# Performance work log

Hardware: AMD Instinct MI355X
Metric: run time of the kernel (lower is better)

## Reference

```python
import jax, jax.numpy as jnp
import numpy as np

B, S, D, H = 2, 2048, 1024, 16
HD = D // H
MASK_VALUE = -1000000.0


def setup_inputs() -> dict:
    key = jax.random.key(0)
    ks = jax.random.split(key, 8)
    scale = 1.0 / np.sqrt(D)
    return {
        "Q": jax.random.normal(ks[0], (B, S, D), jnp.float32),
        "K": jax.random.normal(ks[1], (B, S, D), jnp.float32),
        "V": jax.random.normal(ks[2], (B, S, D), jnp.float32),
        "valid_lens": jax.random.randint(ks[3], (B,), 0, S).astype(jnp.int32),
        "Wq": jax.random.normal(ks[4], (D, D), jnp.float32) * scale,
        "Wk": jax.random.normal(ks[5], (D, D), jnp.float32) * scale,
        "Wv": jax.random.normal(ks[6], (D, D), jnp.float32) * scale,
        "Wo": jax.random.normal(ks[7], (D, D), jnp.float32) * scale,
    }


def _split_heads(x):
    # [B,S,D] -> [B,H,S,HD]
    return x.reshape(B, S, H, HD).transpose(0, 2, 1, 3)


def reference(Q, K, V, valid_lens, Wq, Wk, Wv, Wo):
    q = _split_heads(Q @ Wq)
    k = _split_heads(K @ Wk)
    v = _split_heads(V @ Wv)
    # scores: [B,H,Sq,Sk]
    scores = jnp.einsum("bhqd,bhkd->bhqk", q, k) / jnp.sqrt(jnp.float32(HD))
    # mask key positions >= valid_len (per batch, broadcast over heads/queries)
    key_pos = jnp.arange(S)  # [Sk]
    mask = key_pos[None, None, None, :] < valid_lens[:, None, None, None]
    scores = jnp.where(mask, scores, MASK_VALUE)
    attn = jax.nn.softmax(scores, axis=-1)
    out = jnp.einsum("bhqk,bhkd->bhqd", attn, v)  # [B,H,S,HD]
    out = out.transpose(0, 2, 1, 3).reshape(B, S, D)
    return out @ Wo
```

## Files before the change

kernel.cpp:

```cpp
#include <hip/hip_runtime.h>
#include <stdint.h>

#define B_ 2
#define S_ 2048
#define D_ 1024
#define H_ 16
#define HD_ 64
#define MG_ (B_*S_)
#define MASKV -1000000.0f
#define LP_ 72
#define LO_ 68
#define M2_ 17.3f

typedef __bf16 bf16;
typedef bf16 bf16x8 __attribute__((ext_vector_type(8)));
typedef bf16 bf16x4 __attribute__((ext_vector_type(4)));
typedef float f32x4 __attribute__((ext_vector_type(4)));

#define MFMA(a, b, c) __builtin_amdgcn_mfma_f32_16x16x32_bf16(a, b, c, 0, 0, 0)

__device__ __forceinline__ void gl_lds16(const bf16* g, bf16* l) {
  __builtin_amdgcn_global_load_lds((const __attribute__((address_space(1))) void*)g,
                                   (__attribute__((address_space(3))) void*)l, 16, 0, 0);
}

__global__ __launch_bounds__(256) void wcast_kernel(const float* __restrict__ W0, const float* __restrict__ W1,
                                                    const float* __restrict__ W2, const float* __restrict__ W3,
                                                    bf16* __restrict__ T) {
  const float* W = blockIdx.z == 0 ? W0 : blockIdx.z == 1 ? W1 : blockIdx.z == 2 ? W2 : W3;
  bf16* Tz = T + (size_t)blockIdx.z * D_ * D_;
  __shared__ float tile[32][33];
  int tx = threadIdx.x & 31, ty = threadIdx.x >> 5;
  int bn = blockIdx.x * 32, bk = blockIdx.y * 32;
#pragma unroll
  for (int i = 0; i < 32; i += 8)
    tile[ty + i][tx] = W[(size_t)(bk + ty + i) * D_ + bn + tx];
  __syncthreads();
#pragma unroll
  for (int i = 0; i < 32; i += 8)
    Tz[(size_t)(bn + ty + i) * D_ + bk + tx] = (bf16)tile[tx][ty + i];
}

__global__ __launch_bounds__(256) void proj_gemm(const float* __restrict__ Qin, const float* __restrict__ Kin,
                                                 const float* __restrict__ Vin, const bf16* __restrict__ WT,
                                                 bf16* __restrict__ qh, bf16* __restrict__ kh,
                                                 bf16* __restrict__ vT) {
  __shared__ alignas(16) bf16 Asf[128 * 32];
  __shared__ alignas(16) bf16 Ash[128 * 32];
  int mode = blockIdx.y;
  int bx = blockIdx.x;
  int i1 = (bx & 7) + ((bx >> 6) << 3);
  int i2 = (bx >> 3) & 7;
  int tid = threadIdx.x, lane = tid & 63, w = tid >> 6;
  int wm = w >> 1, wn = w & 1, ml = lane & 15, quad = lane >> 4;
  int rr = tid >> 3, c4 = (tid & 7) * 4;
  int l4 = lane >> 2, k8 = (lane & 3) * 8;
  f32x4 acc[4][4] = {};

  const float* Fp = mode == 0 ? Qin : mode == 1 ? Kin : Vin;
  const bf16* Hp = WT + (size_t)mode * D_ * D_;
  int frow0 = i1 * 128, hrow0 = i2 * 128;
  bf16* Xs = (mode < 2) ? Asf : Ash;
  bf16* Ys = (mode < 2) ? Ash : Asf;

  for (int kk = 0; kk < D_; kk += 32) {
    __syncthreads();
#pragma unroll
    for (int j = 0; j < 2; ++j) {
      int chunk = w * 2 + j;
      gl_lds16(&Hp[(size_t)(hrow0 + chunk * 16 + l4) * D_ + kk + k8], &Ash[chunk * 16 * 32]);
    }
#pragma unroll
    for (int p = 0; p < 4; ++p) {
      float4 v = *(const float4*)&Fp[(size_t)(frow0 + rr + p * 32) * D_ + kk + c4];
      bf16x4 bv; bv[0] = (bf16)v.x; bv[1] = (bf16)v.y; bv[2] = (bf16)v.z; bv[3] = (bf16)v.w;
      *(bf16x4*)&Asf[(rr + p * 32) * 32 + c4] = bv;
    }
    __syncthreads();
    bf16x8 af[4], bfr[4];
#pragma unroll
    for (int mt = 0; mt < 4; ++mt) af[mt] = *(bf16x8*)&Xs[(wm * 64 + mt * 16 + ml) * 32 + quad * 8];
#pragma unroll
    for (int nt = 0; nt < 4; ++nt) bfr[nt] = *(bf16x8*)&Ys[(wn * 64 + nt * 16 + ml) * 32 + quad * 8];
#pragma unroll
    for (int mt = 0; mt < 4; ++mt)
#pragma unroll
      for (int nt = 0; nt < 4; ++nt)
        acc[mt][nt] = MFMA(af[mt], bfr[nt], acc[mt][nt]);
  }

  if (mode < 2) {
    bf16* dst = mode ? kh : qh;
    float oscale = mode ? 1.0f : 0.125f * 1.44269504088896f;
    int m0 = i1 * 128, n0 = i2 * 128;
#pragma unroll
    for (int mt = 0; mt < 4; ++mt)
#pragma unroll
      for (int nt = 0; nt < 4; ++nt)
#pragma unroll
        for (int r = 0; r < 4; ++r) {
          int m = m0 + wm * 64 + mt * 16 + quad * 4 + r;
          int n = n0 + wn * 64 + nt * 16 + ml;
          int b = m >> 11, s = m & (S_ - 1), h = n >> 6, hd = n & 63;
          dst[(((size_t)(b * H_ + h)) * S_ + s) * HD_ + hd] = (bf16)(acc[mt][nt][r] * oscale);
        }
  } else {
    int m0 = i2 * 128, n0 = i1 * 128;
#pragma unroll
    for (int mt = 0; mt < 4; ++mt)
#pragma unroll
      for (int nt = 0; nt < 4; ++nt)
#pragma unroll
        for (int r = 0; r < 4; ++r) {
          int dcol = m0 + wm * 64 + mt * 16 + quad * 4 + r;
          int n = n0 + wn * 64 + nt * 16 + ml;
          int b = n >> 11, s = n & (S_ - 1), h = dcol >> 6, hd = dcol & 63;
          vT[(((size_t)(b * H_ + h)) * HD_ + hd) * S_ + s] = (bf16)acc[mt][nt][r];
        }
  }
}

__global__ __launch_bounds__(256) void attn_kernel(const bf16* __restrict__ qh, const bf16* __restrict__ kh,
                                                   const bf16* __restrict__ vT, const int* __restrict__ vlen,
                                                   bf16* __restrict__ ctx) {
  __shared__ alignas(16) char ldsraw[35328];
  bf16* Ps = (bf16*)ldsraw;
  float* Om = (float*)ldsraw;
  float* Lv = (float*)(ldsraw + 34816);

  int tid = threadIdx.x, lane = tid & 63, w = tid >> 6;
  int ml = lane & 15, quad = lane >> 4;
  int wq = w >> 1, wk = w & 1;
  int bx = blockIdx.x;
  int bh = (bx & 7) + ((bx >> 8) << 3);
  int qt = (bx >> 3) & 31;
  int b = bh >> 4, h = bh & 15;
  const bf16* qbase = qh + ((size_t)bh * S_ + qt * 64 + wq * 32) * HD_;
  const bf16* kbase = kh + (size_t)bh * S_ * HD_;
  const bf16* vbase = vT + (size_t)bh * HD_ * S_;
  int valid = vlen[b];
  int nkt = (valid == 0) ? (S_ / 64) : ((valid + 63) >> 6);

  bf16x8 aq[2][2];
#pragma unroll
  for (int mt = 0; mt < 2; ++mt)
#pragma unroll
    for (int half = 0; half < 2; ++half)
      aq[mt][half] = *(const bf16x8*)&qbase[(mt * 16 + ml) * HD_ + half * 32 + quad * 8];

  bf16 onev = (bf16)1.0f;
  bf16x8 ones = {onev, onev, onev, onev, onev, onev, onev, onev};

  f32x4 o[2][4] = {};
  f32x4 lacc[2] = {};

  bf16* Pw = Ps + (size_t)w * 32 * LP_;

  for (int kt = wk; kt < nkt; kt += 2) {
    const bf16* kp = kbase + (size_t)kt * 64 * HD_;
    bool tail = (kt * 64 + 64 > valid);
    bf16x8 bk[4][2];
#pragma unroll
    for (int nt = 0; nt < 4; ++nt)
#pragma unroll
      for (int half = 0; half < 2; ++half)
        bk[nt][half] = *(const bf16x8*)&kp[(nt * 16 + ml) * HD_ + half * 32 + quad * 8];

#pragma unroll
    for (int mt = 0; mt < 2; ++mt) {
      f32x4 sc[4];
#pragma unroll
      for (int nt = 0; nt < 4; ++nt) {
        f32x4 c = {};
        c = MFMA(aq[mt][0], bk[nt][0], c);
        c = MFMA(aq[mt][1], bk[nt][1], c);
        sc[nt] = c;
      }
#pragma unroll
      for (int r = 0; r < 4; ++r) {
#pragma unroll
        for (int nt = 0; nt < 4; ++nt) {
          float s = sc[nt][r];
          if (tail) {
            int col = kt * 64 + nt * 16 + ml;
            if (col >= valid) s = MASKV;
          }
          if (valid == 0) s = 0.f;
          float p = exp2f(s - M2_);
          Pw[(mt * 16 + quad * 4 + r) * LP_ + nt * 16 + ml] = (bf16)p;
        }
      }
    }
#pragma unroll
    for (int ks = 0; ks < 2; ++ks) {
      bf16x8 bv[4];
#pragma unroll
      for (int ht = 0; ht < 4; ++ht)
        bv[ht] = *(const bf16x8*)&vbase[(size_t)(ht * 16 + ml) * S_ + kt * 64 + ks * 32 + quad * 8];
#pragma unroll
      for (int mt = 0; mt < 2; ++mt) {
        bf16x8 ap = *(bf16x8*)&Pw[(mt * 16 + ml) * LP_ + ks * 32 + quad * 8];
        lacc[mt] = MFMA(ap, ones, lacc[mt]);
#pragma unroll
        for (int ht = 0; ht < 4; ++ht) o[mt][ht] = MFMA(ap, bv[ht], o[mt][ht]);
      }
    }
  }

  __syncthreads();
#pragma unroll
  for (int mt = 0; mt < 2; ++mt) {
#pragma unroll
    for (int r = 0; r < 4; ++r) {
      int rl = mt * 16 + quad * 4 + r;
#pragma unroll
      for (int ht = 0; ht < 4; ++ht)
        Om[(w * 32 + rl) * LO_ + ht * 16 + ml] = o[mt][ht][r];
      if (ml == 0) Lv[w * 32 + rl] = lacc[mt][r];
    }
  }
  __syncthreads();
#pragma unroll 4
  for (int rr = 0; rr < 16; ++rr) {
    int rg = w * 16 + rr;
    int wqs = rg >> 5, rl = rg & 31;
    int s0 = (wqs * 2) * 32 + rl, s1 = (wqs * 2 + 1) * 32 + rl;
    float ls = Lv[s0] + Lv[s1];
    float ov = Om[s0 * LO_ + lane] + Om[s1 * LO_ + lane];
    ctx[((size_t)b * S_ + qt * 64 + rg) * D_ + h * 64 + lane] = (bf16)(ov / ls);
  }
}

__global__ __launch_bounds__(256) void out_gemm(const bf16* __restrict__ ctx, const bf16* __restrict__ WoT,
                                                float* __restrict__ out) {
  __shared__ alignas(16) bf16 As[128 * 32];
  __shared__ alignas(16) bf16 Bs[64 * 32];
  int bx = blockIdx.x;
  int mt8 = (bx & 7) + ((bx >> 7) << 3);
  int ntile = (bx >> 3) & 15;
  int tid = threadIdx.x, lane = tid & 63, w = tid >> 6;
  int wm = w >> 1, wn = w & 1, ml = lane & 15, quad = lane >> 4;
  int l4 = lane >> 2, k8 = (lane & 3) * 8;
  int m0 = mt8 * 128, n0 = ntile * 64;
  f32x4 acc[4][2] = {};
  for (int kk = 0; kk < D_; kk += 32) {
    __syncthreads();
#pragma unroll
    for (int j = 0; j < 2; ++j) {
      int chunk = w * 2 + j;
      gl_lds16(&ctx[(size_t)(m0 + chunk * 16 + l4) * D_ + kk + k8], &As[chunk * 16 * 32]);
    }
    gl_lds16(&WoT[(size_t)(n0 + w * 16 + l4) * D_ + kk + k8], &Bs[w * 16 * 32]);
    __syncthreads();
    bf16x8 af[4], bfr[2];
#pragma unroll
    for (int mt = 0; mt < 4; ++mt) af[mt] = *(bf16x8*)&As[(wm * 64 + mt * 16 + ml) * 32 + quad * 8];
#pragma unroll
    for (int nt = 0; nt < 2; ++nt) bfr[nt] = *(bf16x8*)&Bs[(wn * 32 + nt * 16 + ml) * 32 + quad * 8];
#pragma unroll
    for (int mt = 0; mt < 4; ++mt)
#pragma unroll
      for (int nt = 0; nt < 2; ++nt)
        acc[mt][nt] = MFMA(af[mt], bfr[nt], acc[mt][nt]);
  }
#pragma unroll
  for (int mt = 0; mt < 4; ++mt)
#pragma unroll
    for (int nt = 0; nt < 2; ++nt)
#pragma unroll
      for (int r = 0; r < 4; ++r) {
        int m = m0 + wm * 64 + mt * 16 + quad * 4 + r;
        int n = n0 + wn * 32 + nt * 16 + ml;
        out[(size_t)m * D_ + n] = acc[mt][nt][r];
      }
}

extern "C" void kernel_launch(void* const* d_in, const int* in_sizes, int n_in,
                              void* d_out, int out_size, void* d_ws, size_t ws_size,
                              hipStream_t stream) {
  const float* Q = (const float*)d_in[0];
  const float* K = (const float*)d_in[1];
  const float* V = (const float*)d_in[2];
  const int* vl = (const int*)d_in[3];
  const float* Wq = (const float*)d_in[4];
  const float* Wk = (const float*)d_in[5];
  const float* Wv = (const float*)d_in[6];
  const float* Wo = (const float*)d_in[7];
  char* ws = (char*)d_ws;
  bf16* WT  = (bf16*)ws;
  bf16* qh  = (bf16*)(ws + 8ull * 1024 * 1024);
  bf16* kh  = (bf16*)(ws + 16ull * 1024 * 1024);
  bf16* vT  = (bf16*)(ws + 24ull * 1024 * 1024);
  bf16* ctx = (bf16*)(ws + 32ull * 1024 * 1024);
  float* out = (float*)d_out;

  wcast_kernel<<<dim3(32, 32, 4), 256, 0, stream>>>(Wq, Wk, Wv, Wo, WT);
  proj_gemm<<<dim3(256, 3), 256, 0, stream>>>(Q, K, V, WT, qh, kh, vT);
  attn_kernel<<<dim3(1024), 256, 0, stream>>>(qh, kh, vT, vl, ctx);
  out_gemm<<<dim3(512), 256, 0, stream>>>(ctx, WT + 3ull * D_ * D_, out);
}
```

Before: 233.2 us.

## Load-balance attention across batches with persistent blocks and 4-way key split

Blocks are split between the two batches in proportion to their valid key-tile counts, and each block loops persistently over (head, 32-row query tile) work units. All four waves now share the same query rows and split the key tiles four ways, with a 4-way LDS reduction at the end of each unit. The intent is to stop blocks for the short-valid batch idling while blocks for the long-valid batch are still running. In exchange the kernel adds extra barriers per work unit and a larger reduction, and it relies on gridDim being chosen by the launcher, which is not shown here.

```diff
diff --git a/kernel.cpp b/kernel.cpp
--- a/kernel.cpp
+++ b/kernel.cpp
@@ -130,104 +130,115 @@
 
   int tid = threadIdx.x, lane = tid & 63, w = tid >> 6;
   int ml = lane & 15, quad = lane >> 4;
-  int wq = w >> 1, wk = w & 1;
+  int wk = w;
+
+  int v0 = vlen[0], v1 = vlen[1];
+  int n0 = (v0 == 0) ? (S_ / 64) : ((v0 + 63) >> 6);
+  int n1 = (v1 == 0) ? (S_ / 64) : ((v1 + 63) >> 6);
+  int G = gridDim.x;
+  int G0 = (int)(((long)G * n0 + ((n0 + n1) >> 1)) / (n0 + n1));
+  G0 = G0 < 1 ? 1 : (G0 > G - 1 ? G - 1 : G0);
   int bx = blockIdx.x;
-  int bh = (bx & 7) + ((bx >> 8) << 3);
-  int qt = (bx >> 3) & 31;
-  int b = bh >> 4, h = bh & 15;
-  const bf16* qbase = qh + ((size_t)bh * S_ + qt * 64 + wq * 32) * HD_;
-  const bf16* kbase = kh + (size_t)bh * S_ * HD_;
-  const bf16* vbase = vT + (size_t)bh * HD_ * S_;
-  int valid = vlen[b];
-  int nkt = (valid == 0) ? (S_ / 64) : ((valid + 63) >> 6);
-
-  bf16x8 aq[2][2];
-#pragma unroll
-  for (int mt = 0; mt < 2; ++mt)
-#pragma unroll
-    for (int half = 0; half < 2; ++half)
-      aq[mt][half] = *(const bf16x8*)&qbase[(mt * 16 + ml) * HD_ + half * 32 + quad * 8];
+  int b, ustart, ustep;
+  if (bx < G0) { b = 0; ustart = bx; ustep = G0; }
+  else         { b = 1; ustart = bx - G0; ustep = G - G0; }
+  int valid = b ? v1 : v0;
+  int nkt = b ? n1 : n0;
 
   bf16 onev = (bf16)1.0f;
   bf16x8 ones = {onev, onev, onev, onev, onev, onev, onev, onev};
-
-  f32x4 o[2][4] = {};
-  f32x4 lacc[2] = {};
-
   bf16* Pw = Ps + (size_t)w * 32 * LP_;
 
-  for (int kt = wk; kt < nkt; kt += 2) {
-    const bf16* kp = kbase + (size_t)kt * 64 * HD_;
-    bool tail = (kt * 64 + 64 > valid);
-    bf16x8 bk[4][2];
-#pragma unroll
-    for (int nt = 0; nt < 4; ++nt)
+  for (int u = ustart; u < 1024; u += ustep) {
+    int h = u & 15, qt = u >> 4;
+    int bh = (b << 4) | h;
+    const bf16* qbase = qh + ((size_t)bh * S_ + qt * 32) * HD_;
+    const bf16* kbase = kh + (size_t)bh * S_ * HD_;
+    const bf16* vbase = vT + (size_t)bh * HD_ * S_;
+
+    bf16x8 aq[2][2];
+#pragma unroll
+    for (int mt = 0; mt < 2; ++mt)
 #pragma unroll
       for (int half = 0; half < 2; ++half)
-        bk[nt][half] = *(const bf16x8*)&kp[(nt * 16 + ml) * HD_ + half * 32 + quad * 8];
-
+        aq[mt][half] = *(const bf16x8*)&qbase[(mt * 16 + ml) * HD_ + half * 32 + quad * 8];
+
+    f32x4 o[2][4] = {};
+    f32x4 lacc[2] = {};
+
+    for (int kt = wk; kt < nkt; kt += 4) {
+      const bf16* kp = kbase + (size_t)kt * 64 * HD_;
+      bool tail = (kt * 64 + 64 > valid);
+      bf16x8 bk[4][2];
+#pragma unroll
+      for (int nt = 0; nt < 4; ++nt)
+#pragma unroll
+        for (int half = 0; half < 2; ++half)
+          bk[nt][half] = *(const bf16x8*)&kp[(nt * 16 + ml) * HD_ + half * 32 + quad * 8];
+
+#pragma unroll
+      for (int mt = 0; mt < 2; ++mt) {
+        f32x4 sc[4];
+#pragma unroll
+        for (int nt = 0; nt < 4; ++nt) {
+          f32x4 c = {};
+          c = MFMA(aq[mt][0], bk[nt][0], c);
+          c = MFMA(aq[mt][1], bk[nt][1], c);
+          sc[nt] = c;
+        }
+#pragma unroll
+        for (int r = 0; r < 4; ++r) {
+#pragma unroll
+          for (int nt = 0; nt < 4; ++nt) {
+            float s = sc[nt][r];
+            if (tail) {
+              int col = kt * 64 + nt * 16 + ml;
+              if (col >= valid) s = MASKV;
+            }
+            if (valid == 0) s = 0.f;
+            float p = exp2f(s - M2_);
+            Pw[(mt * 16 + quad * 4 + r) * LP_ + nt * 16 + ml] = (bf16)p;
+          }
+        }
+      }
+#pragma unroll
+      for (int ks = 0; ks < 2; ++ks) {
+        bf16x8 bv[4];
+#pragma unroll
+        for (int ht = 0; ht < 4; ++ht)
+          bv[ht] = *(const bf16x8*)&vbase[(size_t)(ht * 16 + ml) * S_ + kt * 64 + ks * 32 + quad * 8];
+#pragma unroll
+        for (int mt = 0; mt < 2; ++mt) {
+          bf16x8 ap = *(bf16x8*)&Pw[(mt * 16 + ml) * LP_ + ks * 32 + quad * 8];
+          lacc[mt] = MFMA(ap, ones, lacc[mt]);
+#pragma unroll
+          for (int ht = 0; ht < 4; ++ht) o[mt][ht] = MFMA(ap, bv[ht], o[mt][ht]);
+        }
+      }
+    }
+
+    __syncthreads();
 #pragma unroll
     for (int mt = 0; mt < 2; ++mt) {
-      f32x4 sc[4];
-#pragma unroll
-      for (int nt = 0; nt < 4; ++nt) {
-        f32x4 c = {};
-        c = MFMA(aq[mt][0], bk[nt][0], c);
-        c = MFMA(aq[mt][1], bk[nt][1], c);
-        sc[nt] = c;
+#pragma unroll
+      for (int r = 0; r < 4; ++r) {
+        int rl = mt * 16 + quad * 4 + r;
+#pragma unroll
+        for (int ht = 0; ht < 4; ++ht)
+          Om[(w * 32 + rl) * LO_ + ht * 16 + ml] = o[mt][ht][r];
+        if (ml == 0) Lv[w * 32 + rl] = lacc[mt][r];
       }
-#pragma unroll
-      for (int r = 0; r < 4; ++r) {
-#pragma unroll
-        for (int nt = 0; nt < 4; ++nt) {
-          float s = sc[nt][r];
-          if (tail) {
-            int col = kt * 64 + nt * 16 + ml;
-            if (col >= valid) s = MASKV;
-          }
-          if (valid == 0) s = 0.f;
-          float p = exp2f(s - M2_);
-          Pw[(mt * 16 + quad * 4 + r) * LP_ + nt * 16 + ml] = (bf16)p;
-        }
-      }
-    }
-#pragma unroll
-    for (int ks = 0; ks < 2; ++ks) {
-      bf16x8 bv[4];
-#pragma unroll
-      for (int ht = 0; ht < 4; ++ht)
-        bv[ht] = *(const bf16x8*)&vbase[(size_t)(ht * 16 + ml) * S_ + kt * 64 + ks * 32 + quad * 8];
-#pragma unroll
-      for (int mt = 0; mt < 2; ++mt) {
-        bf16x8 ap = *(bf16x8*)&Pw[(mt * 16 + ml) * LP_ + ks * 32 + quad * 8];
-        lacc[mt] = MFMA(ap, ones, lacc[mt]);
-#pragma unroll
-        for (int ht = 0; ht < 4; ++ht) o[mt][ht] = MFMA(ap, bv[ht], o[mt][ht]);
-      }
-    }
-  }
-
-  __syncthreads();
-#pragma unroll
-  for (int mt = 0; mt < 2; ++mt) {
-#pragma unroll
-    for (int r = 0; r < 4; ++r) {
-      int rl = mt * 16 + quad * 4 + r;
-#pragma unroll
-      for (int ht = 0; ht < 4; ++ht)
-        Om[(w * 32 + rl) * LO_ + ht * 16 + ml] = o[mt][ht][r];
-      if (ml == 0) Lv[w * 32 + rl] = lacc[mt][r];
-    }
-  }
-  __syncthreads();
-#pragma unroll 4
-  for (int rr = 0; rr < 16; ++rr) {
-    int rg = w * 16 + rr;
-    int wqs = rg >> 5, rl = rg & 31;
-    int s0 = (wqs * 2) * 32 + rl, s1 = (wqs * 2 + 1) * 32 + rl;
-    float ls = Lv[s0] + Lv[s1];
-    float ov = Om[s0 * LO_ + lane] + Om[s1 * LO_ + lane];
-    ctx[((size_t)b * S_ + qt * 64 + rg) * D_ + h * 64 + lane] = (bf16)(ov / ls);
+    }
+    __syncthreads();
+#pragma unroll
+    for (int rr = 0; rr < 8; ++rr) {
+      int rl = w * 8 + rr;
+      float ls = Lv[rl] + Lv[32 + rl] + Lv[64 + rl] + Lv[96 + rl];
+      float ov = Om[rl * LO_ + lane] + Om[(32 + rl) * LO_ + lane] +
+                 Om[(64 + rl) * LO_ + lane] + Om[(96 + rl) * LO_ + lane];
+      ctx[((size_t)b * S_ + qt * 32 + rl) * D_ + h * 64 + lane] = (bf16)(ov / ls);
+    }
+    __syncthreads();
   }
 }
 
```

New measurement: 283.7 us. +21.6%, slower.

## Skip K/V projection tiles beyond valid length and async-load fp32 tokens

Applied to the files above, without the earlier changes.

The K and V projection GEMM blocks now return early when their token rows lie past the rounded-up valid length, since attention never reads those keys or values. The fp32 token tiles are loaded straight into LDS with global_load_lds and converted to bf16 when the MFMA fragments are read, replacing the register load, convert and LDS store path. The valid==0 case now zeroes Q fragments instead of doing a per-element branch in the softmax loop. This cuts projection work in proportion to the padding and shortens the load path, at the cost of twice the LDS for the fp32 tile and extra conversion work during fragment reads.

```diff
diff --git a/kernel.cpp b/kernel.cpp
--- a/kernel.cpp
+++ b/kernel.cpp
@@ -11,6 +11,7 @@
 #define LP_ 72
 #define LO_ 68
 #define M2_ 17.3f
+#define QSCALE_ (0.125f * 1.44269504088896f)
 
 typedef __bf16 bf16;
 typedef bf16 bf16x8 __attribute__((ext_vector_type(8)));
@@ -19,9 +20,22 @@
 
 #define MFMA(a, b, c) __builtin_amdgcn_mfma_f32_16x16x32_bf16(a, b, c, 0, 0, 0)
 
-__device__ __forceinline__ void gl_lds16(const bf16* g, bf16* l) {
+__device__ __forceinline__ void gl_lds16(const void* g, void* l) {
   __builtin_amdgcn_global_load_lds((const __attribute__((address_space(1))) void*)g,
                                    (__attribute__((address_space(3))) void*)l, 16, 0, 0);
+}
+
+__device__ __forceinline__ bf16x8 ldcvt8(const float* p) {
+  float4 a = *(const float4*)p;
+  float4 b = *(const float4*)(p + 4);
+  bf16x8 r;
+  r[0] = (bf16)a.x; r[1] = (bf16)a.y; r[2] = (bf16)a.z; r[3] = (bf16)a.w;
+  r[4] = (bf16)b.x; r[5] = (bf16)b.y; r[6] = (bf16)b.z; r[7] = (bf16)b.w;
+  return r;
+}
+
+__device__ __forceinline__ int kneed_of(int valid) {
+  return (valid == 0) ? S_ : ((valid + 63) & ~63);
 }
 
 __global__ __launch_bounds__(256) void wcast_kernel(const float* __restrict__ W0, const float* __restrict__ W1,
@@ -44,44 +58,53 @@
 __global__ __launch_bounds__(256) void proj_gemm(const float* __restrict__ Qin, const float* __restrict__ Kin,
                                                  const float* __restrict__ Vin, const bf16* __restrict__ WT,
                                                  bf16* __restrict__ qh, bf16* __restrict__ kh,
-                                                 bf16* __restrict__ vT) {
-  __shared__ alignas(16) bf16 Asf[128 * 32];
-  __shared__ alignas(16) bf16 Ash[128 * 32];
+                                                 bf16* __restrict__ vT, const int* __restrict__ vlen) {
+  __shared__ alignas(16) float Sf[128 * 32];
+  __shared__ alignas(16) bf16 Sw[128 * 32];
   int mode = blockIdx.y;
   int bx = blockIdx.x;
   int i1 = (bx & 7) + ((bx >> 6) << 3);
   int i2 = (bx >> 3) & 7;
+  if (mode >= 1) {
+    int m0tok = i1 * 128;
+    int b = m0tok >> 11, s0 = m0tok & (S_ - 1);
+    if (s0 >= kneed_of(vlen[b])) return;
+  }
   int tid = threadIdx.x, lane = tid & 63, w = tid >> 6;
   int wm = w >> 1, wn = w & 1, ml = lane & 15, quad = lane >> 4;
-  int rr = tid >> 3, c4 = (tid & 7) * 4;
   int l4 = lane >> 2, k8 = (lane & 3) * 8;
+  int l8 = lane >> 3, f4 = (lane & 7) * 4;
   f32x4 acc[4][4] = {};
 
-  const float* Fp = mode == 0 ? Qin : mode == 1 ? Kin : Vin;
+  const float* Tok = mode == 0 ? Qin : mode == 1 ? Kin : Vin;
   const bf16* Hp = WT + (size_t)mode * D_ * D_;
   int frow0 = i1 * 128, hrow0 = i2 * 128;
-  bf16* Xs = (mode < 2) ? Asf : Ash;
-  bf16* Ys = (mode < 2) ? Ash : Asf;
 
   for (int kk = 0; kk < D_; kk += 32) {
     __syncthreads();
 #pragma unroll
+    for (int j = 0; j < 4; ++j) {
+      int chunk = w * 4 + j;
+      gl_lds16(&Tok[(size_t)(frow0 + chunk * 8 + l8) * D_ + kk + f4], &Sf[chunk * 256]);
+    }
+#pragma unroll
     for (int j = 0; j < 2; ++j) {
       int chunk = w * 2 + j;
-      gl_lds16(&Hp[(size_t)(hrow0 + chunk * 16 + l4) * D_ + kk + k8], &Ash[chunk * 16 * 32]);
-    }
-#pragma unroll
-    for (int p = 0; p < 4; ++p) {
-      float4 v = *(const float4*)&Fp[(size_t)(frow0 + rr + p * 32) * D_ + kk + c4];
-      bf16x4 bv; bv[0] = (bf16)v.x; bv[1] = (bf16)v.y; bv[2] = (bf16)v.z; bv[3] = (bf16)v.w;
-      *(bf16x4*)&Asf[(rr + p * 32) * 32 + c4] = bv;
+      gl_lds16(&Hp[(size_t)(hrow0 + chunk * 16 + l4) * D_ + kk + k8], &Sw[chunk * 16 * 32]);
     }
     __syncthreads();
     bf16x8 af[4], bfr[4];
-#pragma unroll
-    for (int mt = 0; mt < 4; ++mt) af[mt] = *(bf16x8*)&Xs[(wm * 64 + mt * 16 + ml) * 32 + quad * 8];
-#pragma unroll
-    for (int nt = 0; nt < 4; ++nt) bfr[nt] = *(bf16x8*)&Ys[(wn * 64 + nt * 16 + ml) * 32 + quad * 8];
+    if (mode < 2) {
+#pragma unroll
+      for (int mt = 0; mt < 4; ++mt) af[mt] = ldcvt8(&Sf[(wm * 64 + mt * 16 + ml) * 32 + quad * 8]);
+#pragma unroll
+      for (int nt = 0; nt < 4; ++nt) bfr[nt] = *(bf16x8*)&Sw[(wn * 64 + nt * 16 + ml) * 32 + quad * 8];
+    } else {
+#pragma unroll
+      for (int mt = 0; mt < 4; ++mt) af[mt] = *(bf16x8*)&Sw[(wm * 64 + mt * 16 + ml) * 32 + quad * 8];
+#pragma unroll
+      for (int nt = 0; nt < 4; ++nt) bfr[nt] = ldcvt8(&Sf[(wn * 64 + nt * 16 + ml) * 32 + quad * 8]);
+    }
 #pragma unroll
     for (int mt = 0; mt < 4; ++mt)
 #pragma unroll
@@ -91,7 +114,7 @@
 
   if (mode < 2) {
     bf16* dst = mode ? kh : qh;
-    float oscale = mode ? 1.0f : 0.125f * 1.44269504088896f;
+    float oscale = mode ? 1.0f : QSCALE_;
     int m0 = i1 * 128, n0 = i2 * 128;
 #pragma unroll
     for (int mt = 0; mt < 4; ++mt)
@@ -147,6 +170,13 @@
 #pragma unroll
     for (int half = 0; half < 2; ++half)
       aq[mt][half] = *(const bf16x8*)&qbase[(mt * 16 + ml) * HD_ + half * 32 + quad * 8];
+  if (valid == 0) {
+    bf16x8 z = {};
+#pragma unroll
+    for (int mt = 0; mt < 2; ++mt)
+#pragma unroll
+      for (int half = 0; half < 2; ++half) aq[mt][half] = z;
+  }
 
   bf16 onev = (bf16)1.0f;
   bf16x8 ones = {onev, onev, onev, onev, onev, onev, onev, onev};
@@ -158,7 +188,7 @@
 
   for (int kt = wk; kt < nkt; kt += 2) {
     const bf16* kp = kbase + (size_t)kt * 64 * HD_;
-    bool tail = (kt * 64 + 64 > valid);
+    bool tail = (valid != 0) && (kt * 64 + 64 > valid);
     bf16x8 bk[4][2];
 #pragma unroll
     for (int nt = 0; nt < 4; ++nt)
@@ -185,7 +215,6 @@
             int col = kt * 64 + nt * 16 + ml;
             if (col >= valid) s = MASKV;
           }
-          if (valid == 0) s = 0.f;
           float p = exp2f(s - M2_);
           Pw[(mt * 16 + quad * 4 + r) * LP_ + nt * 16 + ml] = (bf16)p;
         }
@@ -295,7 +324,7 @@
   float* out = (float*)d_out;
 
   wcast_kernel<<<dim3(32, 32, 4), 256, 0, stream>>>(Wq, Wk, Wv, Wo, WT);
-  proj_gemm<<<dim3(256, 3), 256, 0, stream>>>(Q, K, V, WT, qh, kh, vT);
+  proj_gemm<<<dim3(256, 3), 256, 0, stream>>>(Q, K, V, WT, qh, kh, vT, vl);
   attn_kernel<<<dim3(1024), 256, 0, stream>>>(qh, kh, vT, vl, ctx);
   out_gemm<<<dim3(512), 256, 0, stream>>>(ctx, WT + 3ull * D_ * D_, out);
 }
```

After: 248.7 us. 1.07x slower.
